# Performance work log

Measured on AMD Instinct MI355X. Metric: run time of the kernel, lower is better.

The kernel has to match this reference:

```python
import jax, jax.numpy as jnp
import numpy as np

N = 50000
H = 128          # hidden/in/out channels
F = 128          # num_filters
R = 64           # num_rbf
E = 1_600_000    # graph edges
K = 3            # discrete kernel size
RC = 5.0         # cutoff radius


def setup_inputs() -> dict:
    key = jax.random.key(0)
    ks = jax.random.split(key, 16)
    x = jax.random.normal(ks[0], (N, H), dtype=jnp.float32)
    edge_index = jax.random.randint(ks[1], (2, E), 0, N)
    edge_weight = jax.random.uniform(ks[2], (E,), dtype=jnp.float32) * RC
    edge_attr = jax.random.normal(ks[3], (E, R), dtype=jnp.float32)
    # sequential +/-1 neighbor edges (get_seq_neigh): src-dst in {+1,-1}
    i = jnp.arange(N - 1)
    src = jnp.concatenate([i + 1, i])
    dst = jnp.concatenate([i, i + 1])
    disc_edge_index = jnp.stack([src, dst])  # (2, 2*(N-1))

    def xavier(k, shape):
        fan_in, fan_out = shape[1], shape[0]
        lim = jnp.sqrt(6.0 / (fan_in + fan_out)).astype(jnp.float32)
        return jax.random.uniform(k, shape, jnp.float32, -lim, lim)

    return {
        "x": x,
        "edge_weight": edge_weight,
        "edge_attr": edge_attr,
        # filter network: Linear(R,F) -> tanh -> Linear(F,F)
        "fw1": xavier(ks[4], (F, R)), "fb1": jnp.zeros((F,), jnp.float32),
        "fw2": xavier(ks[5], (F, F)), "fb2": jnp.zeros((F,), jnp.float32),
        "lin1_w": xavier(ks[6], (F, H)),                 # no bias
        "lin2_w": xavier(ks[7], (H, F)), "lin2_b": jnp.zeros((H,), jnp.float32),
        "disc_w": xavier(ks[8], (K, F)),                 # DiscConv weight
        "lin_w": xavier(ks[9], (H, H)), "lin_b": jnp.zeros((H,), jnp.float32),
        "edge_index": edge_index,
        "disc_edge_index": disc_edge_index,
    }


def reference(x, edge_weight, edge_attr, fw1, fb1, fw2, fb2,
              lin1_w, lin2_w, lin2_b, disc_w, lin_w, lin_b,
              edge_index, disc_edge_index):
    n = x.shape[0]
    # cosine cutoff envelope
    C = 0.5 * (jnp.cos(edge_weight * (jnp.pi / RC)) + 1.0)
    C = jnp.where(edge_weight < RC, C, 0.0)
    # filter network on expanded distances
    W = jnp.tanh(edge_attr @ fw1.T + fb1) @ fw2.T + fb2
    W = W * C[:, None]                                   # (E, F)
    # lin1 (no bias)
    h = x @ lin1_w.T                                     # (N, F)
    # gather-multiply-scatter message passing
    src, dst = edge_index[0], edge_index[1]
    msg = h[src] * W                                     # (E, F)
    agg = jax.ops.segment_sum(msg, dst, num_segments=n)  # (N, F)
    # discrete sequential convolution (DiscConv)
    dsrc, ddst = disc_edge_index[0], disc_edge_index[1]
    widx = jnp.mod(dsrc - ddst, K)                       # torch weight[-1] == weight[K-1]
    dmsg = disc_w[widx] * h[dsrc]
    disc_out = jax.ops.segment_sum(dmsg, ddst, num_segments=n) + disc_w[0] * h
    h = agg + disc_out
    # lin2 -> tanh -> interaction-block lin
    h = h @ lin2_w.T + lin2_b
    h = jnp.tanh(h)
    return h @ lin_w.T + lin_b
```

## Files before the change

### kernel.cpp

```cpp
#include <hip/hip_runtime.h>
#include <math.h>

#define HD 128
#define FD 128
#define RD 64
#define TE 128
#define RC_CUT 5.0f

typedef _Float16 half8_t __attribute__((ext_vector_type(8)));
typedef float floatx4 __attribute__((ext_vector_type(4)));

__device__ __forceinline__ float fast_tanh(float x) {
    float ex = __expf(2.0f * x);
    return 1.0f - 2.0f / (ex + 1.0f);
}

__global__ __launch_bounds__(256) void lin1_kernel(const float* __restrict__ x,
                                                   const float* __restrict__ w,
                                                   float* __restrict__ h, int n)
{
    __shared__ float sx[16][HD];
    int base = blockIdx.x * 16;
    for (int i = threadIdx.x; i < 16 * HD; i += 256) {
        int r = i >> 7, c = i & 127;
        int row = base + r;
        sx[r][c] = (row < n) ? x[(size_t)row * HD + c] : 0.0f;
    }
    __syncthreads();
    int f = threadIdx.x & 127;
    int half = threadIdx.x >> 7;
    float acc[8];
#pragma unroll
    for (int r = 0; r < 8; ++r) acc[r] = 0.0f;
    const float* wrow = w + (size_t)f * HD;
    for (int k = 0; k < HD; ++k) {
        float wv = wrow[k];
#pragma unroll
        for (int r = 0; r < 8; ++r) acc[r] += sx[half * 8 + r][k] * wv;
    }
#pragma unroll
    for (int r = 0; r < 8; ++r) {
        int row = base + half * 8 + r;
        if (row < n) h[(size_t)row * FD + f] = acc[r];
    }
}

__global__ __launch_bounds__(256) void count_kernel(const int* __restrict__ dstp,
                                                    int* cnt, int E)
{
    for (int e = blockIdx.x * blockDim.x + threadIdx.x; e < E;
         e += gridDim.x * blockDim.x)
        atomicAdd(&cnt[dstp[e]], 1);
}

__global__ __launch_bounds__(256) void scan1_kernel(const int* __restrict__ cnt,
                                                    int* bsum, int n)
{
    int i = blockIdx.x * 256 + threadIdx.x;
    int v = (i < n) ? cnt[i] : 0;
    int lane = threadIdx.x & 63;
    int wv = threadIdx.x >> 6;
    int s = v;
#pragma unroll
    for (int d = 1; d < 64; d <<= 1) s += __shfl_xor(s, d);
    __shared__ int ws[4];
    if (lane == 0) ws[wv] = s;
    __syncthreads();
    if (threadIdx.x == 0) bsum[blockIdx.x] = ws[0] + ws[1] + ws[2] + ws[3];
}

__global__ void scan2_kernel(int* bsum, int nb, int* totalp)
{
    int lane = threadIdx.x;
    int carry = 0;
    for (int base = 0; base < nb; base += 64) {
        int i = base + lane;
        int v = (i < nb) ? bsum[i] : 0;
        int orig = v;
#pragma unroll
        for (int d = 1; d < 64; d <<= 1) {
            int t = __shfl_up(v, d);
            if (lane >= d) v += t;
        }
        if (i < nb) bsum[i] = carry + v - orig;
        carry += __shfl(v, 63);
    }
    if (lane == 0) *totalp = carry;
}

__global__ __launch_bounds__(256) void scan3_kernel(int* cnt, const int* __restrict__ bsum,
                                                    int* offs, int n)
{
    int i = blockIdx.x * 256 + threadIdx.x;
    int v = (i < n) ? cnt[i] : 0;
    int lane = threadIdx.x & 63;
    int wv = threadIdx.x >> 6;
    int incl = v;
#pragma unroll
    for (int d = 1; d < 64; d <<= 1) {
        int t = __shfl_up(incl, d);
        if (lane >= d) incl += t;
    }
    __shared__ int ws[4];
    if (lane == 63) ws[wv] = incl;
    __syncthreads();
    int wbase = 0;
#pragma unroll
    for (int w = 0; w < 4; ++w) wbase += (w < wv) ? ws[w] : 0;
    int excl = bsum[blockIdx.x] + wbase + incl - v;
    if (i < n) { offs[i] = excl; cnt[i] = excl; }
}

__global__ __launch_bounds__(256) void scatter_kernel(
    const int* __restrict__ srcp, const int* __restrict__ dstp,
    int* cursor, int* __restrict__ inv, unsigned int* __restrict__ meta, int E)
{
    for (int e = blockIdx.x * blockDim.x + threadIdx.x; e < E;
         e += gridDim.x * blockDim.x) {
        int d = dstp[e];
        int p = atomicAdd(&cursor[d], 1);
        inv[e] = p;
        meta[p] = (unsigned int)srcp[e] | ((unsigned int)d << 16);
    }
}

__device__ __forceinline__ half8_t lds_read8(const char* base, int row,
                                             int rowstride, int col) {
    int off = row * rowstride + ((col * 2) ^ ((row & 7) << 4));
    return *(const half8_t*)(base + off);
}

__global__ __launch_bounds__(1024, 8) void edge_gemm_kernel(
    const float* __restrict__ edge_weight,
    const float* __restrict__ edge_attr,
    const float* __restrict__ fw1, const float* __restrict__ fb1,
    const float* __restrict__ fw2, const float* __restrict__ fb2,
    const int* __restrict__ inv,
    _Float16* __restrict__ Wp,
    int E, int ntiles)
{
    extern __shared__ char smem[];
    char* sT  = smem;
    char* sB1 = smem + 32768;
    char* sB2 = smem + 49152;

    for (int i = threadIdx.x * 8; i < FD * RD; i += blockDim.x * 8) {
        int r = i >> 6, c = i & 63;
        const float4* g = (const float4*)(fw1 + (size_t)r * RD + c);
        float4 v0 = g[0], v1 = g[1];
        half8_t hv;
        hv[0] = (_Float16)v0.x; hv[1] = (_Float16)v0.y;
        hv[2] = (_Float16)v0.z; hv[3] = (_Float16)v0.w;
        hv[4] = (_Float16)v1.x; hv[5] = (_Float16)v1.y;
        hv[6] = (_Float16)v1.z; hv[7] = (_Float16)v1.w;
        *(half8_t*)(sB1 + r * 128 + ((c * 2) ^ ((r & 7) << 4))) = hv;
    }
    for (int i = threadIdx.x * 8; i < FD * FD; i += blockDim.x * 8) {
        int r = i >> 7, c = i & 127;
        const float4* g = (const float4*)(fw2 + (size_t)r * FD + c);
        float4 v0 = g[0], v1 = g[1];
        half8_t hv;
        hv[0] = (_Float16)v0.x; hv[1] = (_Float16)v0.y;
        hv[2] = (_Float16)v0.z; hv[3] = (_Float16)v0.w;
        hv[4] = (_Float16)v1.x; hv[5] = (_Float16)v1.y;
        hv[6] = (_Float16)v1.z; hv[7] = (_Float16)v1.w;
        *(half8_t*)(sB2 + r * 256 + ((c * 2) ^ ((r & 7) << 4))) = hv;
    }

    int lane = threadIdx.x & 63;
    int wid  = threadIdx.x >> 6;
    int wm = wid >> 2;
    int wn = wid & 3;
    int l15 = lane & 15;
    int l4  = lane >> 4;

    float bias1[2], bias2[2];
    int gcol[2];
#pragma unroll
    for (int ni = 0; ni < 2; ++ni) {
        gcol[ni]  = wn * 32 + ni * 16 + l15;
        bias1[ni] = fb1[gcol[ni]];
        bias2[ni] = fb2[gcol[ni]];
    }

    int pr = threadIdx.x >> 3;
    int pc = (threadIdx.x & 7) * 8;

    float4 pA0 = {0.f, 0.f, 0.f, 0.f}, pA1 = {0.f, 0.f, 0.f, 0.f};
    {
        int e = blockIdx.x * TE + pr;
        if (e < E) {
            const float4* g = (const float4*)(edge_attr + (size_t)e * RD + pc);
            pA0 = g[0]; pA1 = g[1];
        }
    }
    __syncthreads();

    for (int tile = blockIdx.x; tile < ntiles; tile += gridDim.x) {
        int e0 = tile * TE;
        {
            half8_t hv;
            hv[0] = (_Float16)pA0.x; hv[1] = (_Float16)pA0.y;
            hv[2] = (_Float16)pA0.z; hv[3] = (_Float16)pA0.w;
            hv[4] = (_Float16)pA1.x; hv[5] = (_Float16)pA1.y;
            hv[6] = (_Float16)pA1.z; hv[7] = (_Float16)pA1.w;
            *(half8_t*)(sT + pr * 128 + ((pc * 2) ^ ((pr & 7) << 4))) = hv;
        }
        __syncthreads();

        {
            int nt = tile + gridDim.x;
            pA0 = (float4){0.f, 0.f, 0.f, 0.f};
            pA1 = (float4){0.f, 0.f, 0.f, 0.f};
            if (nt < ntiles) {
                int e = nt * TE + pr;
                if (e < E) {
                    const float4* g = (const float4*)(edge_attr + (size_t)e * RD + pc);
                    pA0 = g[0]; pA1 = g[1];
                }
            }
        }

        floatx4 acc[2][2];
#pragma unroll
        for (int mi = 0; mi < 2; ++mi)
#pragma unroll
            for (int ni = 0; ni < 2; ++ni)
                acc[mi][ni] = (floatx4){0.f, 0.f, 0.f, 0.f};
#pragma unroll
        for (int ks = 0; ks < 2; ++ks) {
            int k = ks * 32 + l4 * 8;
            half8_t a[2], b[2];
#pragma unroll
            for (int mi = 0; mi < 2; ++mi)
                a[mi] = lds_read8(sT, wm * 32 + mi * 16 + l15, 128, k);
#pragma unroll
            for (int ni = 0; ni < 2; ++ni)
                b[ni] = lds_read8(sB1, wn * 32 + ni * 16 + l15, 128, k);
#pragma unroll
            for (int mi = 0; mi < 2; ++mi)
#pragma unroll
                for (int ni = 0; ni < 2; ++ni)
                    acc[mi][ni] = __builtin_amdgcn_mfma_f32_16x16x32_f16(
                        a[mi], b[ni], acc[mi][ni], 0, 0, 0);
        }
        __syncthreads();

#pragma unroll
        for (int ni = 0; ni < 2; ++ni) {
            int f = gcol[ni];
            float bias = bias1[ni];
#pragma unroll
            for (int mi = 0; mi < 2; ++mi) {
#pragma unroll
                for (int j = 0; j < 4; ++j) {
                    int e = wm * 32 + mi * 16 + l4 * 4 + j;
                    float t = fast_tanh(acc[mi][ni][j] + bias);
                    *(_Float16*)(sT + e * 256 + ((f * 2) ^ ((e & 7) << 4))) =
                        (_Float16)t;
                }
            }
        }
        __syncthreads();

        floatx4 acc2[2][2];
#pragma unroll
        for (int mi = 0; mi < 2; ++mi)
#pragma unroll
            for (int ni = 0; ni < 2; ++ni)
                acc2[mi][ni] = (floatx4){0.f, 0.f, 0.f, 0.f};
#pragma unroll
        for (int ks = 0; ks < 4; ++ks) {
            int k = ks * 32 + l4 * 8;
            half8_t a[2], b[2];
#pragma unroll
            for (int mi = 0; mi < 2; ++mi)
                a[mi] = lds_read8(sT, wm * 32 + mi * 16 + l15, 256, k);
#pragma unroll
            for (int ni = 0; ni < 2; ++ni)
                b[ni] = lds_read8(sB2, wn * 32 + ni * 16 + l15, 256, k);
#pragma unroll
            for (int mi = 0; mi < 2; ++mi)
#pragma unroll
                for (int ni = 0; ni < 2; ++ni)
                    acc2[mi][ni] = __builtin_amdgcn_mfma_f32_16x16x32_f16(
                        a[mi], b[ni], acc2[mi][ni], 0, 0, 0);
        }
        __syncthreads();

#pragma unroll
        for (int mi = 0; mi < 2; ++mi) {
            float d4[4];
#pragma unroll
            for (int j = 0; j < 4; ++j) {
                int el = wm * 32 + mi * 16 + l4 * 4 + j;
                int idx = (e0 + el < E) ? (e0 + el) : (E - 1);
                d4[j] = edge_weight[idx];
            }
#pragma unroll
            for (int j = 0; j < 4; ++j) {
                int el = wm * 32 + mi * 16 + l4 * 4 + j;
                float C = (d4[j] < RC_CUT)
                            ? 0.5f * (__cosf(d4[j] * 0.6283185307179586f) + 1.0f)
                            : 0.0f;
#pragma unroll
                for (int ni = 0; ni < 2; ++ni) {
                    int f = gcol[ni];
                    float wv = (acc2[mi][ni][j] + bias2[ni]) * C;
                    *(_Float16*)(sT + el * 256 + ((f * 2) ^ ((el & 7) << 4))) =
                        (_Float16)wv;
                }
            }
        }
        __syncthreads();

#pragma unroll
        for (int k = 0; k < 2; ++k) {
            int t = threadIdx.x + k * 1024;
            int r = t >> 4, ch = t & 15;
            int e = e0 + r;
            if (e < E) {
                half8_t v = lds_read8(sT, r, 256, ch * 8);
                int pv = inv[e];
                *(half8_t*)(Wp + (size_t)pv * FD + ch * 8) = v;
            }
        }
        __syncthreads();
    }
}

__global__ __launch_bounds__(256) void agg_kernel(
    const _Float16* __restrict__ Wp,
    const unsigned int* __restrict__ meta,
    const int* __restrict__ offs,
    const float* __restrict__ h,
    float* __restrict__ agg, int n)
{
    int g = (blockIdx.x * 256 + (int)threadIdx.x) >> 4;
    if (g >= n) return;
    int lg = threadIdx.x & 15;
    int p  = offs[g];
    int p1 = offs[g + 1];

    float acc[8];
#pragma unroll
    for (int q = 0; q < 8; ++q) acc[q] = 0.0f;

    for (; p + 2 <= p1; p += 2) {
        int s0 = (int)(meta[p] & 0xFFFFu);
        int s1 = (int)(meta[p + 1] & 0xFFFFu);
        half8_t w0 = *(const half8_t*)(Wp + (size_t)p * FD + lg * 8);
        half8_t w1 = *(const half8_t*)(Wp + (size_t)(p + 1) * FD + lg * 8);
        const float4* ha = (const float4*)(h + (size_t)s0 * FD + lg * 8);
        const float4* hb = (const float4*)(h + (size_t)s1 * FD + lg * 8);
        float4 a0 = ha[0], a1 = ha[1];
        float4 b0 = hb[0], b1 = hb[1];
        acc[0] += (float)w0[0] * a0.x + (float)w1[0] * b0.x;
        acc[1] += (float)w0[1] * a0.y + (float)w1[1] * b0.y;
        acc[2] += (float)w0[2] * a0.z + (float)w1[2] * b0.z;
        acc[3] += (float)w0[3] * a0.w + (float)w1[3] * b0.w;
        acc[4] += (float)w0[4] * a1.x + (float)w1[4] * b1.x;
        acc[5] += (float)w0[5] * a1.y + (float)w1[5] * b1.y;
        acc[6] += (float)w0[6] * a1.z + (float)w1[6] * b1.z;
        acc[7] += (float)w0[7] * a1.w + (float)w1[7] * b1.w;
    }
    if (p < p1) {
        int s0 = (int)(meta[p] & 0xFFFFu);
        half8_t w0 = *(const half8_t*)(Wp + (size_t)p * FD + lg * 8);
        const float4* ha = (const float4*)(h + (size_t)s0 * FD + lg * 8);
        float4 a0 = ha[0], a1 = ha[1];
        acc[0] += (float)w0[0] * a0.x;
        acc[1] += (float)w0[1] * a0.y;
        acc[2] += (float)w0[2] * a0.z;
        acc[3] += (float)w0[3] * a0.w;
        acc[4] += (float)w0[4] * a1.x;
        acc[5] += (float)w0[5] * a1.y;
        acc[6] += (float)w0[6] * a1.z;
        acc[7] += (float)w0[7] * a1.w;
    }
    float* ar = agg + (size_t)g * FD + lg * 8;
    *(float4*)ar       = (float4){acc[0], acc[1], acc[2], acc[3]};
    *(float4*)(ar + 4) = (float4){acc[4], acc[5], acc[6], acc[7]};
}

__global__ __launch_bounds__(1024, 8) void edge_kernel_atomic(
    const float* __restrict__ edge_weight,
    const float* __restrict__ edge_attr,
    const float* __restrict__ fw1, const float* __restrict__ fb1,
    const float* __restrict__ fw2, const float* __restrict__ fb2,
    const int* __restrict__ eidx,
    const float* __restrict__ h,
    float* agg, int E, int ntiles)
{
    extern __shared__ char smem[];
    char* sT  = smem;
    char* sB1 = smem + 32768;
    char* sB2 = smem + 49152;

    for (int i = threadIdx.x * 8; i < FD * RD; i += blockDim.x * 8) {
        int r = i >> 6, c = i & 63;
        const float4* g = (const float4*)(fw1 + (size_t)r * RD + c);
        float4 v0 = g[0], v1 = g[1];
        half8_t hv;
        hv[0] = (_Float16)v0.x; hv[1] = (_Float16)v0.y;
        hv[2] = (_Float16)v0.z; hv[3] = (_Float16)v0.w;
        hv[4] = (_Float16)v1.x; hv[5] = (_Float16)v1.y;
        hv[6] = (_Float16)v1.z; hv[7] = (_Float16)v1.w;
        *(half8_t*)(sB1 + r * 128 + ((c * 2) ^ ((r & 7) << 4))) = hv;
    }
    for (int i = threadIdx.x * 8; i < FD * FD; i += blockDim.x * 8) {
        int r = i >> 7, c = i & 127;
        const float4* g = (const float4*)(fw2 + (size_t)r * FD + c);
        float4 v0 = g[0], v1 = g[1];
        half8_t hv;
        hv[0] = (_Float16)v0.x; hv[1] = (_Float16)v0.y;
        hv[2] = (_Float16)v0.z; hv[3] = (_Float16)v0.w;
        hv[4] = (_Float16)v1.x; hv[5] = (_Float16)v1.y;
        hv[6] = (_Float16)v1.z; hv[7] = (_Float16)v1.w;
        *(half8_t*)(sB2 + r * 256 + ((c * 2) ^ ((r & 7) << 4))) = hv;
    }
    __syncthreads();

    const int* srcp = eidx;
    const int* dstp = eidx + E;
    int lane = threadIdx.x & 63;
    int wid  = threadIdx.x >> 6;
    int wm = wid >> 2;
    int wn = wid & 3;
    int l15 = lane & 15;
    int l4  = lane >> 4;

    for (int tile = blockIdx.x; tile < ntiles; tile += gridDim.x) {
        int e0 = tile * TE;
        for (int i = threadIdx.x * 8; i < TE * RD; i += blockDim.x * 8) {
            int r = i >> 6, c = i & 63;
            half8_t hv;
            if (e0 + r < E) {
                const float4* g = (const float4*)(edge_attr + (size_t)(e0 + r) * RD + c);
                float4 v0 = g[0], v1 = g[1];
                hv[0] = (_Float16)v0.x; hv[1] = (_Float16)v0.y;
                hv[2] = (_Float16)v0.z; hv[3] = (_Float16)v0.w;
                hv[4] = (_Float16)v1.x; hv[5] = (_Float16)v1.y;
                hv[6] = (_Float16)v1.z; hv[7] = (_Float16)v1.w;
            } else {
                for (int q = 0; q < 8; ++q) hv[q] = (_Float16)0.0f;
            }
            *(half8_t*)(sT + r * 128 + ((c * 2) ^ ((r & 7) << 4))) = hv;
        }
        __syncthreads();

        floatx4 acc[2][2];
#pragma unroll
        for (int mi = 0; mi < 2; ++mi)
#pragma unroll
            for (int ni = 0; ni < 2; ++ni)
                acc[mi][ni] = (floatx4){0.f, 0.f, 0.f, 0.f};
#pragma unroll
        for (int ks = 0; ks < 2; ++ks) {
            int k = ks * 32 + l4 * 8;
            half8_t a[2], b[2];
#pragma unroll
            for (int mi = 0; mi < 2; ++mi)
                a[mi] = lds_read8(sT, wm * 32 + mi * 16 + l15, 128, k);
#pragma unroll
            for (int ni = 0; ni < 2; ++ni)
                b[ni] = lds_read8(sB1, wn * 32 + ni * 16 + l15, 128, k);
#pragma unroll
            for (int mi = 0; mi < 2; ++mi)
#pragma unroll
                for (int ni = 0; ni < 2; ++ni)
                    acc[mi][ni] = __builtin_amdgcn_mfma_f32_16x16x32_f16(
                        a[mi], b[ni], acc[mi][ni], 0, 0, 0);
        }
        __syncthreads();

#pragma unroll
        for (int ni = 0; ni < 2; ++ni) {
            int f = wn * 32 + ni * 16 + l15;
            float bias = fb1[f];
#pragma unroll
            for (int mi = 0; mi < 2; ++mi) {
#pragma unroll
                for (int j = 0; j < 4; ++j) {
                    int e = wm * 32 + mi * 16 + l4 * 4 + j;
                    float t = fast_tanh(acc[mi][ni][j] + bias);
                    *(_Float16*)(sT + e * 256 + ((f * 2) ^ ((e & 7) << 4))) =
                        (_Float16)t;
                }
            }
        }
        __syncthreads();

        floatx4 acc2[2][2];
#pragma unroll
        for (int mi = 0; mi < 2; ++mi)
#pragma unroll
            for (int ni = 0; ni < 2; ++ni)
                acc2[mi][ni] = (floatx4){0.f, 0.f, 0.f, 0.f};
#pragma unroll
        for (int ks = 0; ks < 4; ++ks) {
            int k = ks * 32 + l4 * 8;
            half8_t a[2], b[2];
#pragma unroll
            for (int mi = 0; mi < 2; ++mi)
                a[mi] = lds_read8(sT, wm * 32 + mi * 16 + l15, 256, k);
#pragma unroll
            for (int ni = 0; ni < 2; ++ni)
                b[ni] = lds_read8(sB2, wn * 32 + ni * 16 + l15, 256, k);
#pragma unroll
            for (int mi = 0; mi < 2; ++mi)
#pragma unroll
                for (int ni = 0; ni < 2; ++ni)
                    acc2[mi][ni] = __builtin_amdgcn_mfma_f32_16x16x32_f16(
                        a[mi], b[ni], acc2[mi][ni], 0, 0, 0);
        }
        __syncthreads();

        float bias2[2];
        int gcol[2];
#pragma unroll
        for (int ni = 0; ni < 2; ++ni) {
            gcol[ni] = wn * 32 + ni * 16 + l15;
            bias2[ni] = fb2[gcol[ni]];
        }
#pragma unroll
        for (int mi = 0; mi < 2; ++mi) {
            int ge[4], s4[4], dn4[4];
            float d4[4];
#pragma unroll
            for (int j = 0; j < 4; ++j) {
                int el = wm * 32 + mi * 16 + l4 * 4 + j;
                ge[j] = e0 + el;
                int idx = (ge[j] < E) ? ge[j] : (E - 1);
                s4[j]  = srcp[idx];
                dn4[j] = dstp[idx];
                d4[j]  = edge_weight[idx];
            }
#pragma unroll
            for (int j = 0; j < 4; ++j) {
                if (ge[j] >= E) continue;
                float C = (d4[j] < RC_CUT)
                            ? 0.5f * (__cosf(d4[j] * 0.6283185307179586f) + 1.0f)
                            : 0.0f;
                const float* hrow = h + (size_t)s4[j] * FD;
                float* ar = agg + (size_t)dn4[j] * FD;
#pragma unroll
                for (int ni = 0; ni < 2; ++ni) {
                    int g = gcol[ni];
                    float wv = (acc2[mi][ni][j] + bias2[ni]) * C;
                    atomicAdd(ar + g, wv * hrow[g]);
                }
            }
        }
    }
}

__global__ __launch_bounds__(256) void final_kernel(
    const float* aggin, const float* __restrict__ h,
    const float* __restrict__ disc_w,
    const float* __restrict__ lin2_w, const float* __restrict__ lin2_b,
    const float* __restrict__ lin_w, const float* __restrict__ lin_b,
    float* out, int n)
{
    __shared__ float sg[16][FD];
    __shared__ float sm[16][FD];
    int base = blockIdx.x * 16;
    for (int i = threadIdx.x; i < 16 * FD; i += 256) {
        int r = i >> 7, c = i & 127;
        int row = base + r;
        float v = 0.0f;
        if (row < n) {
            v = aggin[(size_t)row * FD + c] + disc_w[c] * h[(size_t)row * FD + c];
            if (row + 1 < n) v += disc_w[FD + c] * h[(size_t)(row + 1) * FD + c];
            if (row >= 1)    v += disc_w[2 * FD + c] * h[(size_t)(row - 1) * FD + c];
        }
        sg[r][c] = v;
    }
    __syncthreads();
    int f = threadIdx.x & 127;
    int half = threadIdx.x >> 7;
    {
        float acc[8];
        float b = lin2_b[f];
#pragma unroll
        for (int r = 0; r < 8; ++r) acc[r] = b;
        const float* wrow = lin2_w + (size_t)f * FD;
        for (int k = 0; k < FD; ++k) {
            float wv = wrow[k];
#pragma unroll
            for (int r = 0; r < 8; ++r) acc[r] += sg[half * 8 + r][k] * wv;
        }
#pragma unroll
        for (int r = 0; r < 8; ++r) sm[half * 8 + r][f] = fast_tanh(acc[r]);
    }
    __syncthreads();
    {
        float acc[8];
        float b = lin_b[f];
#pragma unroll
        for (int r = 0; r < 8; ++r) acc[r] = b;
        const float* wrow = lin_w + (size_t)f * HD;
        for (int k = 0; k < FD; ++k) {
            float wv = wrow[k];
#pragma unroll
            for (int r = 0; r < 8; ++r) acc[r] += sm[half * 8 + r][k] * wv;
        }
#pragma unroll
        for (int r = 0; r < 8; ++r) {
            int row = base + half * 8 + r;
            if (row < n) out[(size_t)row * HD + f] = acc[r];
        }
    }
}

extern "C" void kernel_launch(void* const* d_in, const int* in_sizes, int n_in,
                              void* d_out, int out_size, void* d_ws, size_t ws_size,
                              hipStream_t stream)
{
    const float* x      = (const float*)d_in[0];
    const float* ew     = (const float*)d_in[1];
    const float* ea     = (const float*)d_in[2];
    const float* fw1    = (const float*)d_in[3];
    const float* fb1    = (const float*)d_in[4];
    const float* fw2    = (const float*)d_in[5];
    const float* fb2    = (const float*)d_in[6];
    const float* lin1_w = (const float*)d_in[7];
    const float* lin2_w = (const float*)d_in[8];
    const float* lin2_b = (const float*)d_in[9];
    const float* disc_w = (const float*)d_in[10];
    const float* lin_w  = (const float*)d_in[11];
    const float* lin_b  = (const float*)d_in[12];
    const int*   eidx   = (const int*)d_in[13];

    int n = in_sizes[0] / HD;
    int E = in_sizes[1];
    int ntiles = (E + TE - 1) / TE;
    int nb = (n + 255) / 256;
    float* out = (float*)d_out;

    const int* srcp = eidx;
    const int* dstp = eidx + E;

    char* base = (char*)d_ws;
    float*     h    = (float*)base;
    size_t off_h    = (size_t)n * FD * 4;
    _Float16*  Wp   = (_Float16*)(base + off_h);
    size_t off_w    = off_h + (size_t)E * FD * 2;
    int*       inv  = (int*)(base + off_w);
    size_t off_i    = off_w + (size_t)E * 4;
    unsigned int* meta = (unsigned int*)(base + off_i);
    size_t off_m    = off_i + (size_t)E * 4;
    int*       cnt  = (int*)(base + off_m);
    int*       offs = cnt + n;
    int*       bsum = offs + n + 1;
    size_t need     = off_m + (size_t)(2 * n + nb + 16) * 4;

    hipMemsetAsync(d_out, 0, (size_t)out_size * sizeof(float), stream);
    lin1_kernel<<<(n + 15) / 16, 256, 0, stream>>>(x, lin1_w, h, n);

    size_t smem = 81920;
    if (ws_size >= need && n <= 65535) {
        hipMemsetAsync(cnt, 0, (size_t)n * sizeof(int), stream);
        count_kernel<<<2048, 256, 0, stream>>>(dstp, cnt, E);
        scan1_kernel<<<nb, 256, 0, stream>>>(cnt, bsum, n);
        scan2_kernel<<<1, 64, 0, stream>>>(bsum, nb, offs + n);
        scan3_kernel<<<nb, 256, 0, stream>>>(cnt, bsum, offs, n);
        scatter_kernel<<<2048, 256, 0, stream>>>(srcp, dstp, cnt, inv, meta, E);

        hipFuncSetAttribute((const void*)edge_gemm_kernel,
                            hipFuncAttributeMaxDynamicSharedMemorySize, (int)smem);
        int nblocks = ntiles < 512 ? ntiles : 512;
        edge_gemm_kernel<<<nblocks, 1024, smem, stream>>>(ew, ea, fw1, fb1, fw2, fb2,
                                                          inv, Wp, E, ntiles);

        int ablocks = (n * 16 + 255) / 256;
        agg_kernel<<<ablocks, 256, 0, stream>>>(Wp, meta, offs, h, out, n);
    } else {
        hipFuncSetAttribute((const void*)edge_kernel_atomic,
                            hipFuncAttributeMaxDynamicSharedMemorySize, (int)smem);
        int nblocks = ntiles < 512 ? ntiles : 512;
        edge_kernel_atomic<<<nblocks, 1024, smem, stream>>>(ew, ea, fw1, fb1, fw2, fb2,
                                                            eidx, h, out, E, ntiles);
    }

    final_kernel<<<(n + 15) / 16, 256, 0, stream>>>(out, h, disc_w, lin2_w, lin2_b,
                                                    lin_w, lin_b, out, n);
}
```

Baseline: 983.0 us.

## Defer edge_attr prefetch, software-pipeline agg gathers, vectorize weight loads

Moves the next-tile edge_attr global prefetch in the edge GEMM kernel to after both MFMA stages, so the load is issued later in each tile iteration. Rewrites the aggregation loop to process four edges per step with double-buffered prefetch of meta and gathered h rows, exposing more memory-level parallelism for the irregular gathers. Vectorizes weight-row reads to float4 in the lin1 and final dense kernels, and skips the output memset on the CSR path, where agg writes every row. The deeper agg prefetch raises register pressure, which could lower occupancy.

```diff
diff --git a/kernel.cpp b/kernel.cpp
--- a/kernel.cpp
+++ b/kernel.cpp
@@ -33,10 +33,15 @@
 #pragma unroll
     for (int r = 0; r < 8; ++r) acc[r] = 0.0f;
     const float* wrow = w + (size_t)f * HD;
-    for (int k = 0; k < HD; ++k) {
-        float wv = wrow[k];
-#pragma unroll
-        for (int r = 0; r < 8; ++r) acc[r] += sx[half * 8 + r][k] * wv;
+    for (int k = 0; k < HD; k += 4) {
+        float4 wv = *(const float4*)(wrow + k);
+#pragma unroll
+        for (int r = 0; r < 8; ++r) {
+            acc[r] += sx[half * 8 + r][k]     * wv.x;
+            acc[r] += sx[half * 8 + r][k + 1] * wv.y;
+            acc[r] += sx[half * 8 + r][k + 2] * wv.z;
+            acc[r] += sx[half * 8 + r][k + 3] * wv.w;
+        }
     }
 #pragma unroll
     for (int r = 0; r < 8; ++r) {
@@ -208,6 +213,98 @@
         }
         __syncthreads();
 
+        floatx4 acc[2][2];
+#pragma unroll
+        for (int mi = 0; mi < 2; ++mi)
+#pragma unroll
+            for (int ni = 0; ni < 2; ++ni)
+                acc[mi][ni] = (floatx4){0.f, 0.f, 0.f, 0.f};
+#pragma unroll
+        for (int ks = 0; ks < 2; ++ks) {
+            int k = ks * 32 + l4 * 8;
+            half8_t a[2], b[2];
+#pragma unroll
+            for (int mi = 0; mi < 2; ++mi)
+                a[mi] = lds_read8(sT, wm * 32 + mi * 16 + l15, 128, k);
+#pragma unroll
+            for (int ni = 0; ni < 2; ++ni)
+                b[ni] = lds_read8(sB1, wn * 32 + ni * 16 + l15, 128, k);
+#pragma unroll
+            for (int mi = 0; mi < 2; ++mi)
+#pragma unroll
+                for (int ni = 0; ni < 2; ++ni)
+                    acc[mi][ni] = __builtin_amdgcn_mfma_f32_16x16x32_f16(
+                        a[mi], b[ni], acc[mi][ni], 0, 0, 0);
+        }
+        __syncthreads();
+
+#pragma unroll
+        for (int ni = 0; ni < 2; ++ni) {
+            int f = gcol[ni];
+            float bias = bias1[ni];
+#pragma unroll
+            for (int mi = 0; mi < 2; ++mi) {
+#pragma unroll
+                for (int j = 0; j < 4; ++j) {
+                    int e = wm * 32 + mi * 16 + l4 * 4 + j;
+                    float t = fast_tanh(acc[mi][ni][j] + bias);
+                    *(_Float16*)(sT + e * 256 + ((f * 2) ^ ((e & 7) << 4))) =
+                        (_Float16)t;
+                }
+            }
+        }
+        __syncthreads();
+
+        floatx4 acc2[2][2];
+#pragma unroll
+        for (int mi = 0; mi < 2; ++mi)
+#pragma unroll
+            for (int ni = 0; ni < 2; ++ni)
+                acc2[mi][ni] = (floatx4){0.f, 0.f, 0.f, 0.f};
+#pragma unroll
+        for (int ks = 0; ks < 4; ++ks) {
+            int k = ks * 32 + l4 * 8;
+            half8_t a[2], b[2];
+#pragma unroll
+            for (int mi = 0; mi < 2; ++mi)
+                a[mi] = lds_read8(sT, wm * 32 + mi * 16 + l15, 256, k);
+#pragma unroll
+            for (int ni = 0; ni < 2; ++ni)
+                b[ni] = lds_read8(sB2, wn * 32 + ni * 16 + l15, 256, k);
+#pragma unroll
+            for (int mi = 0; mi < 2; ++mi)
+#pragma unroll
+                for (int ni = 0; ni < 2; ++ni)
+                    acc2[mi][ni] = __builtin_amdgcn_mfma_f32_16x16x32_f16(
+                        a[mi], b[ni], acc2[mi][ni], 0, 0, 0);
+        }
+        __syncthreads();
+
+#pragma unroll
+        for (int mi = 0; mi < 2; ++mi) {
+            float d4[4];
+#pragma unroll
+            for (int j = 0; j < 4; ++j) {
+                int el = wm * 32 + mi * 16 + l4 * 4 + j;
+                int idx = (e0 + el < E) ? (e0 + el) : (E - 1);
+                d4[j] = edge_weight[idx];
+            }
+#pragma unroll
+            for (int j = 0; j < 4; ++j) {
+                int el = wm * 32 + mi * 16 + l4 * 4 + j;
+                float C = (d4[j] < RC_CUT)
+                            ? 0.5f * (__cosf(d4[j] * 0.6283185307179586f) + 1.0f)
+                            : 0.0f;
+#pragma unroll
+                for (int ni = 0; ni < 2; ++ni) {
+                    int f = gcol[ni];
+                    float wv = (acc2[mi][ni][j] + bias2[ni]) * C;
+                    *(_Float16*)(sT + el * 256 + ((f * 2) ^ ((el & 7) << 4))) =
+                        (_Float16)wv;
+                }
+            }
+        }
+
         {
             int nt = tile + gridDim.x;
             pA0 = (float4){0.f, 0.f, 0.f, 0.f};
@@ -220,98 +317,6 @@
                 }
             }
         }
-
-        floatx4 acc[2][2];
-#pragma unroll
-        for (int mi = 0; mi < 2; ++mi)
-#pragma unroll
-            for (int ni = 0; ni < 2; ++ni)
-                acc[mi][ni] = (floatx4){0.f, 0.f, 0.f, 0.f};
-#pragma unroll
-        for (int ks = 0; ks < 2; ++ks) {
-            int k = ks * 32 + l4 * 8;
-            half8_t a[2], b[2];
-#pragma unroll
-            for (int mi = 0; mi < 2; ++mi)
-                a[mi] = lds_read8(sT, wm * 32 + mi * 16 + l15, 128, k);
-#pragma unroll
-            for (int ni = 0; ni < 2; ++ni)
-                b[ni] = lds_read8(sB1, wn * 32 + ni * 16 + l15, 128, k);
-#pragma unroll
-            for (int mi = 0; mi < 2; ++mi)
-#pragma unroll
-                for (int ni = 0; ni < 2; ++ni)
-                    acc[mi][ni] = __builtin_amdgcn_mfma_f32_16x16x32_f16(
-                        a[mi], b[ni], acc[mi][ni], 0, 0, 0);
-        }
-        __syncthreads();
-
-#pragma unroll
-        for (int ni = 0; ni < 2; ++ni) {
-            int f = gcol[ni];
-            float bias = bias1[ni];
-#pragma unroll
-            for (int mi = 0; mi < 2; ++mi) {
-#pragma unroll
-                for (int j = 0; j < 4; ++j) {
-                    int e = wm * 32 + mi * 16 + l4 * 4 + j;
-                    float t = fast_tanh(acc[mi][ni][j] + bias);
-                    *(_Float16*)(sT + e * 256 + ((f * 2) ^ ((e & 7) << 4))) =
-                        (_Float16)t;
-                }
-            }
-        }
-        __syncthreads();
-
-        floatx4 acc2[2][2];
-#pragma unroll
-        for (int mi = 0; mi < 2; ++mi)
-#pragma unroll
-            for (int ni = 0; ni < 2; ++ni)
-                acc2[mi][ni] = (floatx4){0.f, 0.f, 0.f, 0.f};
-#pragma unroll
-        for (int ks = 0; ks < 4; ++ks) {
-            int k = ks * 32 + l4 * 8;
-            half8_t a[2], b[2];
-#pragma unroll
-            for (int mi = 0; mi < 2; ++mi)
-                a[mi] = lds_read8(sT, wm * 32 + mi * 16 + l15, 256, k);
-#pragma unroll
-            for (int ni = 0; ni < 2; ++ni)
-                b[ni] = lds_read8(sB2, wn * 32 + ni * 16 + l15, 256, k);
-#pragma unroll
-            for (int mi = 0; mi < 2; ++mi)
-#pragma unroll
-                for (int ni = 0; ni < 2; ++ni)
-                    acc2[mi][ni] = __builtin_amdgcn_mfma_f32_16x16x32_f16(
-                        a[mi], b[ni], acc2[mi][ni], 0, 0, 0);
-        }
-        __syncthreads();
-
-#pragma unroll
-        for (int mi = 0; mi < 2; ++mi) {
-            float d4[4];
-#pragma unroll
-            for (int j = 0; j < 4; ++j) {
-                int el = wm * 32 + mi * 16 + l4 * 4 + j;
-                int idx = (e0 + el < E) ? (e0 + el) : (E - 1);
-                d4[j] = edge_weight[idx];
-            }
-#pragma unroll
-            for (int j = 0; j < 4; ++j) {
-                int el = wm * 32 + mi * 16 + l4 * 4 + j;
-                float C = (d4[j] < RC_CUT)
-                            ? 0.5f * (__cosf(d4[j] * 0.6283185307179586f) + 1.0f)
-                            : 0.0f;
-#pragma unroll
-                for (int ni = 0; ni < 2; ++ni) {
-                    int f = gcol[ni];
-                    float wv = (acc2[mi][ni][j] + bias2[ni]) * C;
-                    *(_Float16*)(sT + el * 256 + ((f * 2) ^ ((el & 7) << 4))) =
-                        (_Float16)wv;
-                }
-            }
-        }
         __syncthreads();
 
 #pragma unroll
@@ -329,6 +334,39 @@
     }
 }
 
+#define AGG_PREF(MV, H0, H1, BASE)                                           \
+    {                                                                        \
+        MV##0 = meta[(BASE)];     MV##1 = meta[(BASE) + 1];                  \
+        MV##2 = meta[(BASE) + 2]; MV##3 = meta[(BASE) + 3];                  \
+        const float4* q0 = (const float4*)(h + (size_t)(MV##0 & 0xFFFFu) * FD + lg); \
+        const float4* q1 = (const float4*)(h + (size_t)(MV##1 & 0xFFFFu) * FD + lg); \
+        const float4* q2 = (const float4*)(h + (size_t)(MV##2 & 0xFFFFu) * FD + lg); \
+        const float4* q3 = (const float4*)(h + (size_t)(MV##3 & 0xFFFFu) * FD + lg); \
+        H0[0] = q0[0]; H1[0] = q0[1];                                        \
+        H0[1] = q1[0]; H1[1] = q1[1];                                        \
+        H0[2] = q2[0]; H1[2] = q2[1];                                        \
+        H0[3] = q3[0]; H1[3] = q3[1];                                        \
+    }
+
+#define AGG_STEP(H0, H1, BASE)                                               \
+    {                                                                        \
+        half8_t w_[4];                                                       \
+        _Pragma("unroll")                                                    \
+        for (int u = 0; u < 4; ++u)                                          \
+            w_[u] = *(const half8_t*)(Wp + (size_t)((BASE) + u) * FD + lg);  \
+        _Pragma("unroll")                                                    \
+        for (int u = 0; u < 4; ++u) {                                        \
+            acc[0] += (float)w_[u][0] * H0[u].x;                             \
+            acc[1] += (float)w_[u][1] * H0[u].y;                             \
+            acc[2] += (float)w_[u][2] * H0[u].z;                             \
+            acc[3] += (float)w_[u][3] * H0[u].w;                             \
+            acc[4] += (float)w_[u][4] * H1[u].x;                             \
+            acc[5] += (float)w_[u][5] * H1[u].y;                             \
+            acc[6] += (float)w_[u][6] * H1[u].z;                             \
+            acc[7] += (float)w_[u][7] * H1[u].w;                             \
+        }                                                                    \
+    }
+
 __global__ __launch_bounds__(256) void agg_kernel(
     const _Float16* __restrict__ Wp,
     const unsigned int* __restrict__ meta,
@@ -338,7 +376,7 @@
 {
     int g = (blockIdx.x * 256 + (int)threadIdx.x) >> 4;
     if (g >= n) return;
-    int lg = threadIdx.x & 15;
+    int lg = (threadIdx.x & 15) * 8;
     int p  = offs[g];
     int p1 = offs[g + 1];
 
@@ -346,28 +384,30 @@
 #pragma unroll
     for (int q = 0; q < 8; ++q) acc[q] = 0.0f;
 
-    for (; p + 2 <= p1; p += 2) {
-        int s0 = (int)(meta[p] & 0xFFFFu);
-        int s1 = (int)(meta[p + 1] & 0xFFFFu);
-        half8_t w0 = *(const half8_t*)(Wp + (size_t)p * FD + lg * 8);
-        half8_t w1 = *(const half8_t*)(Wp + (size_t)(p + 1) * FD + lg * 8);
-        const float4* ha = (const float4*)(h + (size_t)s0 * FD + lg * 8);
-        const float4* hb = (const float4*)(h + (size_t)s1 * FD + lg * 8);
-        float4 a0 = ha[0], a1 = ha[1];
-        float4 b0 = hb[0], b1 = hb[1];
-        acc[0] += (float)w0[0] * a0.x + (float)w1[0] * b0.x;
-        acc[1] += (float)w0[1] * a0.y + (float)w1[1] * b0.y;
-        acc[2] += (float)w0[2] * a0.z + (float)w1[2] * b0.z;
-        acc[3] += (float)w0[3] * a0.w + (float)w1[3] * b0.w;
-        acc[4] += (float)w0[4] * a1.x + (float)w1[4] * b1.x;
-        acc[5] += (float)w0[5] * a1.y + (float)w1[5] * b1.y;
-        acc[6] += (float)w0[6] * a1.z + (float)w1[6] * b1.z;
-        acc[7] += (float)w0[7] * a1.w + (float)w1[7] * b1.w;
-    }
-    if (p < p1) {
-        int s0 = (int)(meta[p] & 0xFFFFu);
-        half8_t w0 = *(const half8_t*)(Wp + (size_t)p * FD + lg * 8);
-        const float4* ha = (const float4*)(h + (size_t)s0 * FD + lg * 8);
+    int nfull = (p1 - p) >> 2;
+    int pc = p;
+    unsigned mA0, mA1, mA2, mA3, mB0, mB1, mB2, mB3;
+    float4 A0[4], A1[4], B0[4], B1[4];
+
+    if (nfull > 0) AGG_PREF(mA, A0, A1, pc);
+    int c = 0;
+    for (; c + 2 <= nfull; c += 2) {
+        AGG_PREF(mB, B0, B1, pc + 4);
+        AGG_STEP(A0, A1, pc);
+        pc += 4;
+        if (c + 2 < nfull) AGG_PREF(mA, A0, A1, pc + 4);
+        AGG_STEP(B0, B1, pc);
+        pc += 4;
+    }
+    if (c < nfull) {
+        AGG_STEP(A0, A1, pc);
+        pc += 4;
+    }
+    for (; pc < p1; ++pc) {
+        unsigned m = meta[pc];
+        int s0 = (int)(m & 0xFFFFu);
+        half8_t w0 = *(const half8_t*)(Wp + (size_t)pc * FD + lg);
+        const float4* ha = (const float4*)(h + (size_t)s0 * FD + lg);
         float4 a0 = ha[0], a1 = ha[1];
         acc[0] += (float)w0[0] * a0.x;
         acc[1] += (float)w0[1] * a0.y;
@@ -378,7 +418,7 @@
         acc[6] += (float)w0[6] * a1.z;
         acc[7] += (float)w0[7] * a1.w;
     }
-    float* ar = agg + (size_t)g * FD + lg * 8;
+    float* ar = agg + (size_t)g * FD + lg;
     *(float4*)ar       = (float4){acc[0], acc[1], acc[2], acc[3]};
     *(float4*)(ar + 4) = (float4){acc[4], acc[5], acc[6], acc[7]};
 }
@@ -585,10 +625,15 @@
 #pragma unroll
         for (int r = 0; r < 8; ++r) acc[r] = b;
         const float* wrow = lin2_w + (size_t)f * FD;
-        for (int k = 0; k < FD; ++k) {
-            float wv = wrow[k];
-#pragma unroll
-            for (int r = 0; r < 8; ++r) acc[r] += sg[half * 8 + r][k] * wv;
+        for (int k = 0; k < FD; k += 4) {
+            float4 wv = *(const float4*)(wrow + k);
+#pragma unroll
+            for (int r = 0; r < 8; ++r) {
+                acc[r] += sg[half * 8 + r][k]     * wv.x;
+                acc[r] += sg[half * 8 + r][k + 1] * wv.y;
+                acc[r] += sg[half * 8 + r][k + 2] * wv.z;
+                acc[r] += sg[half * 8 + r][k + 3] * wv.w;
+            }
         }
 #pragma unroll
         for (int r = 0; r < 8; ++r) sm[half * 8 + r][f] = fast_tanh(acc[r]);
@@ -600,10 +645,15 @@
 #pragma unroll
         for (int r = 0; r < 8; ++r) acc[r] = b;
         const float* wrow = lin_w + (size_t)f * HD;
-        for (int k = 0; k < FD; ++k) {
-            float wv = wrow[k];
-#pragma unroll
-            for (int r = 0; r < 8; ++r) acc[r] += sm[half * 8 + r][k] * wv;
+        for (int k = 0; k < FD; k += 4) {
+            float4 wv = *(const float4*)(wrow + k);
+#pragma unroll
+            for (int r = 0; r < 8; ++r) {
+                acc[r] += sm[half * 8 + r][k]     * wv.x;
+                acc[r] += sm[half * 8 + r][k + 1] * wv.y;
+                acc[r] += sm[half * 8 + r][k + 2] * wv.z;
+                acc[r] += sm[half * 8 + r][k + 3] * wv.w;
+            }
         }
 #pragma unroll
         for (int r = 0; r < 8; ++r) {
@@ -655,7 +705,6 @@
     int*       bsum = offs + n + 1;
     size_t need     = off_m + (size_t)(2 * n + nb + 16) * 4;
 
-    hipMemsetAsync(d_out, 0, (size_t)out_size * sizeof(float), stream);
     lin1_kernel<<<(n + 15) / 16, 256, 0, stream>>>(x, lin1_w, h, n);
 
     size_t smem = 81920;
@@ -676,6 +725,7 @@
         int ablocks = (n * 16 + 255) / 256;
         agg_kernel<<<ablocks, 256, 0, stream>>>(Wp, meta, offs, h, out, n);
     } else {
+        hipMemsetAsync(d_out, 0, (size_t)out_size * sizeof(float), stream);
         hipFuncSetAttribute((const void*)edge_kernel_atomic,
                             hipFuncAttributeMaxDynamicSharedMemorySize, (int)smem);
         int nblocks = ntiles < 512 ? ntiles : 512;
```

New measurement: 883.4 us. 1.11x faster.

## Swap MFMA operands to store W directly, widen agg to one wave per node

Applied to the files above, without the earlier changes.

The edge GEMM now passes the MFMA operands in swapped order, so each lane holds four consecutive feature values for one edge. Bias, tanh and the cutoff are applied on those and written as half4 vectors straight to the permuted global Wp, which drops the LDS staging pass and two barriers. The edge_attr prefetch is moved to after the second GEMM. The aggregation kernel now uses one 64-lane wave per node with each lane covering two features, unrolled by four edges, in place of 16 lanes per node. Separately, the lin1 and final GEMMs read weights as float4, and the output memset runs only in the atomic fallback path.

```diff
diff --git a/kernel.cpp b/kernel.cpp
--- a/kernel.cpp
+++ b/kernel.cpp
@@ -8,6 +8,8 @@
 #define RC_CUT 5.0f
 
 typedef _Float16 half8_t __attribute__((ext_vector_type(8)));
+typedef _Float16 half4_t __attribute__((ext_vector_type(4)));
+typedef _Float16 half2_t __attribute__((ext_vector_type(2)));
 typedef float floatx4 __attribute__((ext_vector_type(4)));
 
 __device__ __forceinline__ float fast_tanh(float x) {
@@ -33,10 +35,15 @@
 #pragma unroll
     for (int r = 0; r < 8; ++r) acc[r] = 0.0f;
     const float* wrow = w + (size_t)f * HD;
-    for (int k = 0; k < HD; ++k) {
-        float wv = wrow[k];
-#pragma unroll
-        for (int r = 0; r < 8; ++r) acc[r] += sx[half * 8 + r][k] * wv;
+    for (int k = 0; k < HD; k += 4) {
+        float4 wv = *(const float4*)(wrow + k);
+#pragma unroll
+        for (int r = 0; r < 8; ++r) {
+            acc[r] += sx[half * 8 + r][k]     * wv.x;
+            acc[r] += sx[half * 8 + r][k + 1] * wv.y;
+            acc[r] += sx[half * 8 + r][k + 2] * wv.z;
+            acc[r] += sx[half * 8 + r][k + 3] * wv.w;
+        }
     }
 #pragma unroll
     for (int r = 0; r < 8; ++r) {
@@ -174,14 +181,9 @@
     int l15 = lane & 15;
     int l4  = lane >> 4;
 
-    float bias1[2], bias2[2];
-    int gcol[2];
-#pragma unroll
-    for (int ni = 0; ni < 2; ++ni) {
-        gcol[ni]  = wn * 32 + ni * 16 + l15;
-        bias1[ni] = fb1[gcol[ni]];
-        bias2[ni] = fb2[gcol[ni]];
-    }
+    int fbase[2];
+#pragma unroll
+    for (int ni = 0; ni < 2; ++ni) fbase[ni] = wn * 32 + ni * 16 + l4 * 4;
 
     int pr = threadIdx.x >> 3;
     int pc = (threadIdx.x & 7) * 8;
@@ -207,6 +209,71 @@
             *(half8_t*)(sT + pr * 128 + ((pc * 2) ^ ((pr & 7) << 4))) = hv;
         }
         __syncthreads();
+
+        floatx4 acc[2][2];
+#pragma unroll
+        for (int mi = 0; mi < 2; ++mi)
+#pragma unroll
+            for (int ni = 0; ni < 2; ++ni)
+                acc[mi][ni] = (floatx4){0.f, 0.f, 0.f, 0.f};
+#pragma unroll
+        for (int ks = 0; ks < 2; ++ks) {
+            int k = ks * 32 + l4 * 8;
+            half8_t a[2], b[2];
+#pragma unroll
+            for (int mi = 0; mi < 2; ++mi)
+                a[mi] = lds_read8(sT, wm * 32 + mi * 16 + l15, 128, k);
+#pragma unroll
+            for (int ni = 0; ni < 2; ++ni)
+                b[ni] = lds_read8(sB1, wn * 32 + ni * 16 + l15, 128, k);
+#pragma unroll
+            for (int mi = 0; mi < 2; ++mi)
+#pragma unroll
+                for (int ni = 0; ni < 2; ++ni)
+                    acc[mi][ni] = __builtin_amdgcn_mfma_f32_16x16x32_f16(
+                        b[ni], a[mi], acc[mi][ni], 0, 0, 0);
+        }
+        __syncthreads();
+
+#pragma unroll
+        for (int ni = 0; ni < 2; ++ni) {
+            float4 bv = *(const float4*)(fb1 + fbase[ni]);
+#pragma unroll
+            for (int mi = 0; mi < 2; ++mi) {
+                int e = wm * 32 + mi * 16 + l15;
+                half4_t hv;
+                hv[0] = (_Float16)fast_tanh(acc[mi][ni][0] + bv.x);
+                hv[1] = (_Float16)fast_tanh(acc[mi][ni][1] + bv.y);
+                hv[2] = (_Float16)fast_tanh(acc[mi][ni][2] + bv.z);
+                hv[3] = (_Float16)fast_tanh(acc[mi][ni][3] + bv.w);
+                *(half4_t*)(sT + e * 256 + ((fbase[ni] * 2) ^ ((e & 7) << 4))) = hv;
+            }
+        }
+        __syncthreads();
+
+        floatx4 acc2[2][2];
+#pragma unroll
+        for (int mi = 0; mi < 2; ++mi)
+#pragma unroll
+            for (int ni = 0; ni < 2; ++ni)
+                acc2[mi][ni] = (floatx4){0.f, 0.f, 0.f, 0.f};
+#pragma unroll
+        for (int ks = 0; ks < 4; ++ks) {
+            int k = ks * 32 + l4 * 8;
+            half8_t a[2], b[2];
+#pragma unroll
+            for (int mi = 0; mi < 2; ++mi)
+                a[mi] = lds_read8(sT, wm * 32 + mi * 16 + l15, 256, k);
+#pragma unroll
+            for (int ni = 0; ni < 2; ++ni)
+                b[ni] = lds_read8(sB2, wn * 32 + ni * 16 + l15, 256, k);
+#pragma unroll
+            for (int mi = 0; mi < 2; ++mi)
+#pragma unroll
+                for (int ni = 0; ni < 2; ++ni)
+                    acc2[mi][ni] = __builtin_amdgcn_mfma_f32_16x16x32_f16(
+                        b[ni], a[mi], acc2[mi][ni], 0, 0, 0);
+        }
 
         {
             int nt = tile + gridDim.x;
@@ -221,108 +288,27 @@
             }
         }
 
-        floatx4 acc[2][2];
-#pragma unroll
-        for (int mi = 0; mi < 2; ++mi)
-#pragma unroll
-            for (int ni = 0; ni < 2; ++ni)
-                acc[mi][ni] = (floatx4){0.f, 0.f, 0.f, 0.f};
-#pragma unroll
-        for (int ks = 0; ks < 2; ++ks) {
-            int k = ks * 32 + l4 * 8;
-            half8_t a[2], b[2];
-#pragma unroll
-            for (int mi = 0; mi < 2; ++mi)
-                a[mi] = lds_read8(sT, wm * 32 + mi * 16 + l15, 128, k);
-#pragma unroll
-            for (int ni = 0; ni < 2; ++ni)
-                b[ni] = lds_read8(sB1, wn * 32 + ni * 16 + l15, 128, k);
-#pragma unroll
-            for (int mi = 0; mi < 2; ++mi)
-#pragma unroll
-                for (int ni = 0; ni < 2; ++ni)
-                    acc[mi][ni] = __builtin_amdgcn_mfma_f32_16x16x32_f16(
-                        a[mi], b[ni], acc[mi][ni], 0, 0, 0);
-        }
-        __syncthreads();
-
-#pragma unroll
-        for (int ni = 0; ni < 2; ++ni) {
-            int f = gcol[ni];
-            float bias = bias1[ni];
-#pragma unroll
-            for (int mi = 0; mi < 2; ++mi) {
-#pragma unroll
-                for (int j = 0; j < 4; ++j) {
-                    int e = wm * 32 + mi * 16 + l4 * 4 + j;
-                    float t = fast_tanh(acc[mi][ni][j] + bias);
-                    *(_Float16*)(sT + e * 256 + ((f * 2) ^ ((e & 7) << 4))) =
-                        (_Float16)t;
+#pragma unroll
+        for (int mi = 0; mi < 2; ++mi) {
+            int el = wm * 32 + mi * 16 + l15;
+            int ge = e0 + el;
+            int idx = (ge < E) ? ge : (E - 1);
+            float d = edge_weight[idx];
+            int pv = inv[idx];
+            float C = (d < RC_CUT)
+                        ? 0.5f * (__cosf(d * 0.6283185307179586f) + 1.0f)
+                        : 0.0f;
+            if (ge < E) {
+#pragma unroll
+                for (int ni = 0; ni < 2; ++ni) {
+                    float4 bv = *(const float4*)(fb2 + fbase[ni]);
+                    half4_t hv;
+                    hv[0] = (_Float16)((acc2[mi][ni][0] + bv.x) * C);
+                    hv[1] = (_Float16)((acc2[mi][ni][1] + bv.y) * C);
+                    hv[2] = (_Float16)((acc2[mi][ni][2] + bv.z) * C);
+                    hv[3] = (_Float16)((acc2[mi][ni][3] + bv.w) * C);
+                    *(half4_t*)(Wp + (size_t)pv * FD + fbase[ni]) = hv;
                 }
-            }
-        }
-        __syncthreads();
-
-        floatx4 acc2[2][2];
-#pragma unroll
-        for (int mi = 0; mi < 2; ++mi)
-#pragma unroll
-            for (int ni = 0; ni < 2; ++ni)
-                acc2[mi][ni] = (floatx4){0.f, 0.f, 0.f, 0.f};
-#pragma unroll
-        for (int ks = 0; ks < 4; ++ks) {
-            int k = ks * 32 + l4 * 8;
-            half8_t a[2], b[2];
-#pragma unroll
-            for (int mi = 0; mi < 2; ++mi)
-                a[mi] = lds_read8(sT, wm * 32 + mi * 16 + l15, 256, k);
-#pragma unroll
-            for (int ni = 0; ni < 2; ++ni)
-                b[ni] = lds_read8(sB2, wn * 32 + ni * 16 + l15, 256, k);
-#pragma unroll
-            for (int mi = 0; mi < 2; ++mi)
-#pragma unroll
-                for (int ni = 0; ni < 2; ++ni)
-                    acc2[mi][ni] = __builtin_amdgcn_mfma_f32_16x16x32_f16(
-                        a[mi], b[ni], acc2[mi][ni], 0, 0, 0);
-        }
-        __syncthreads();
-
-#pragma unroll
-        for (int mi = 0; mi < 2; ++mi) {
-            float d4[4];
-#pragma unroll
-            for (int j = 0; j < 4; ++j) {
-                int el = wm * 32 + mi * 16 + l4 * 4 + j;
-                int idx = (e0 + el < E) ? (e0 + el) : (E - 1);
-                d4[j] = edge_weight[idx];
-            }
-#pragma unroll
-            for (int j = 0; j < 4; ++j) {
-                int el = wm * 32 + mi * 16 + l4 * 4 + j;
-                float C = (d4[j] < RC_CUT)
-                            ? 0.5f * (__cosf(d4[j] * 0.6283185307179586f) + 1.0f)
-                            : 0.0f;
-#pragma unroll
-                for (int ni = 0; ni < 2; ++ni) {
-                    int f = gcol[ni];
-                    float wv = (acc2[mi][ni][j] + bias2[ni]) * C;
-                    *(_Float16*)(sT + el * 256 + ((f * 2) ^ ((el & 7) << 4))) =
-                        (_Float16)wv;
-                }
-            }
-        }
-        __syncthreads();
-
-#pragma unroll
-        for (int k = 0; k < 2; ++k) {
-            int t = threadIdx.x + k * 1024;
-            int r = t >> 4, ch = t & 15;
-            int e = e0 + r;
-            if (e < E) {
-                half8_t v = lds_read8(sT, r, 256, ch * 8);
-                int pv = inv[e];
-                *(half8_t*)(Wp + (size_t)pv * FD + ch * 8) = v;
             }
         }
         __syncthreads();
@@ -336,51 +322,38 @@
     const float* __restrict__ h,
     float* __restrict__ agg, int n)
 {
-    int g = (blockIdx.x * 256 + (int)threadIdx.x) >> 4;
+    int g = blockIdx.x * 4 + (threadIdx.x >> 6);
     if (g >= n) return;
-    int lg = threadIdx.x & 15;
+    int lane = threadIdx.x & 63;
     int p  = offs[g];
     int p1 = offs[g + 1];
 
-    float acc[8];
-#pragma unroll
-    for (int q = 0; q < 8; ++q) acc[q] = 0.0f;
-
-    for (; p + 2 <= p1; p += 2) {
-        int s0 = (int)(meta[p] & 0xFFFFu);
-        int s1 = (int)(meta[p + 1] & 0xFFFFu);
-        half8_t w0 = *(const half8_t*)(Wp + (size_t)p * FD + lg * 8);
-        half8_t w1 = *(const half8_t*)(Wp + (size_t)(p + 1) * FD + lg * 8);
-        const float4* ha = (const float4*)(h + (size_t)s0 * FD + lg * 8);
-        const float4* hb = (const float4*)(h + (size_t)s1 * FD + lg * 8);
-        float4 a0 = ha[0], a1 = ha[1];
-        float4 b0 = hb[0], b1 = hb[1];
-        acc[0] += (float)w0[0] * a0.x + (float)w1[0] * b0.x;
-        acc[1] += (float)w0[1] * a0.y + (float)w1[1] * b0.y;
-        acc[2] += (float)w0[2] * a0.z + (float)w1[2] * b0.z;
-        acc[3] += (float)w0[3] * a0.w + (float)w1[3] * b0.w;
-        acc[4] += (float)w0[4] * a1.x + (float)w1[4] * b1.x;
-        acc[5] += (float)w0[5] * a1.y + (float)w1[5] * b1.y;
-        acc[6] += (float)w0[6] * a1.z + (float)w1[6] * b1.z;
-        acc[7] += (float)w0[7] * a1.w + (float)w1[7] * b1.w;
-    }
-    if (p < p1) {
-        int s0 = (int)(meta[p] & 0xFFFFu);
-        half8_t w0 = *(const half8_t*)(Wp + (size_t)p * FD + lg * 8);
-        const float4* ha = (const float4*)(h + (size_t)s0 * FD + lg * 8);
-        float4 a0 = ha[0], a1 = ha[1];
-        acc[0] += (float)w0[0] * a0.x;
-        acc[1] += (float)w0[1] * a0.y;
-        acc[2] += (float)w0[2] * a0.z;
-        acc[3] += (float)w0[3] * a0.w;
-        acc[4] += (float)w0[4] * a1.x;
-        acc[5] += (float)w0[5] * a1.y;
-        acc[6] += (float)w0[6] * a1.z;
-        acc[7] += (float)w0[7] * a1.w;
-    }
-    float* ar = agg + (size_t)g * FD + lg * 8;
-    *(float4*)ar       = (float4){acc[0], acc[1], acc[2], acc[3]};
-    *(float4*)(ar + 4) = (float4){acc[4], acc[5], acc[6], acc[7]};
+    float a0 = 0.0f, a1 = 0.0f;
+    const int le = lane * 2;
+
+    for (; p + 4 <= p1; p += 4) {
+        unsigned m0 = meta[p], m1 = meta[p + 1], m2 = meta[p + 2], m3 = meta[p + 3];
+        half2_t w0 = *(const half2_t*)(Wp + (size_t)p * FD + le);
+        half2_t w1 = *(const half2_t*)(Wp + (size_t)(p + 1) * FD + le);
+        half2_t w2 = *(const half2_t*)(Wp + (size_t)(p + 2) * FD + le);
+        half2_t w3 = *(const half2_t*)(Wp + (size_t)(p + 3) * FD + le);
+        float2 h0 = *(const float2*)(h + (size_t)(m0 & 0xFFFFu) * FD + le);
+        float2 h1 = *(const float2*)(h + (size_t)(m1 & 0xFFFFu) * FD + le);
+        float2 h2 = *(const float2*)(h + (size_t)(m2 & 0xFFFFu) * FD + le);
+        float2 h3 = *(const float2*)(h + (size_t)(m3 & 0xFFFFu) * FD + le);
+        a0 += (float)w0[0] * h0.x + (float)w1[0] * h1.x
+            + (float)w2[0] * h2.x + (float)w3[0] * h3.x;
+        a1 += (float)w0[1] * h0.y + (float)w1[1] * h1.y
+            + (float)w2[1] * h2.y + (float)w3[1] * h3.y;
+    }
+    for (; p < p1; ++p) {
+        unsigned m = meta[p];
+        half2_t w = *(const half2_t*)(Wp + (size_t)p * FD + le);
+        float2 hv = *(const float2*)(h + (size_t)(m & 0xFFFFu) * FD + le);
+        a0 += (float)w[0] * hv.x;
+        a1 += (float)w[1] * hv.y;
+    }
+    *(float2*)(agg + (size_t)g * FD + le) = (float2){a0, a1};
 }
 
 __global__ __launch_bounds__(1024, 8) void edge_kernel_atomic(
@@ -585,10 +558,15 @@
 #pragma unroll
         for (int r = 0; r < 8; ++r) acc[r] = b;
         const float* wrow = lin2_w + (size_t)f * FD;
-        for (int k = 0; k < FD; ++k) {
-            float wv = wrow[k];
-#pragma unroll
-            for (int r = 0; r < 8; ++r) acc[r] += sg[half * 8 + r][k] * wv;
+        for (int k = 0; k < FD; k += 4) {
+            float4 wv = *(const float4*)(wrow + k);
+#pragma unroll
+            for (int r = 0; r < 8; ++r) {
+                acc[r] += sg[half * 8 + r][k]     * wv.x;
+                acc[r] += sg[half * 8 + r][k + 1] * wv.y;
+                acc[r] += sg[half * 8 + r][k + 2] * wv.z;
+                acc[r] += sg[half * 8 + r][k + 3] * wv.w;
+            }
         }
 #pragma unroll
         for (int r = 0; r < 8; ++r) sm[half * 8 + r][f] = fast_tanh(acc[r]);
@@ -600,10 +578,15 @@
 #pragma unroll
         for (int r = 0; r < 8; ++r) acc[r] = b;
         const float* wrow = lin_w + (size_t)f * HD;
-        for (int k = 0; k < FD; ++k) {
-            float wv = wrow[k];
-#pragma unroll
-            for (int r = 0; r < 8; ++r) acc[r] += sm[half * 8 + r][k] * wv;
+        for (int k = 0; k < FD; k += 4) {
+            float4 wv = *(const float4*)(wrow + k);
+#pragma unroll
+            for (int r = 0; r < 8; ++r) {
+                acc[r] += sm[half * 8 + r][k]     * wv.x;
+                acc[r] += sm[half * 8 + r][k + 1] * wv.y;
+                acc[r] += sm[half * 8 + r][k + 2] * wv.z;
+                acc[r] += sm[half * 8 + r][k + 3] * wv.w;
+            }
         }
 #pragma unroll
         for (int r = 0; r < 8; ++r) {
@@ -655,7 +638,6 @@
     int*       bsum = offs + n + 1;
     size_t need     = off_m + (size_t)(2 * n + nb + 16) * 4;
 
-    hipMemsetAsync(d_out, 0, (size_t)out_size * sizeof(float), stream);
     lin1_kernel<<<(n + 15) / 16, 256, 0, stream>>>(x, lin1_w, h, n);
 
     size_t smem = 81920;
@@ -673,9 +655,9 @@
         edge_gemm_kernel<<<nblocks, 1024, smem, stream>>>(ew, ea, fw1, fb1, fw2, fb2,
                                                           inv, Wp, E, ntiles);
 
-        int ablocks = (n * 16 + 255) / 256;
-        agg_kernel<<<ablocks, 256, 0, stream>>>(Wp, meta, offs, h, out, n);
+        agg_kernel<<<(n + 3) / 4, 256, 0, stream>>>(Wp, meta, offs, h, out, n);
     } else {
+        hipMemsetAsync(d_out, 0, (size_t)out_size * sizeof(float), stream);
         hipFuncSetAttribute((const void*)edge_kernel_atomic,
                             hipFuncAttributeMaxDynamicSharedMemorySize, (int)smem);
         int nblocks = ntiles < 512 ? ntiles : 512;
```

Measured after the change: 863.5 us. -12.2%, faster.
